# Optimization experiments

Hardware: AMD Instinct MI355X
Metric: run time of the kernel (lower is better)

## Reference

```python
import jax, jax.numpy as jnp
import numpy as np
from jax import lax

B, C, H, W = 8, 128, 48, 48
N = H * W
SPARSITY = 0.8
K_TOP = int(N * SPARSITY)


def conv2d(x, w, b, padding, dilation=1):
    # x: [B,C,H,W], w: [O,I,kh,kw]
    out = lax.conv_general_dilated(
        x, w, window_strides=(1, 1),
        padding=[(padding, padding), (padding, padding)],
        rhs_dilation=(dilation, dilation),
        dimension_numbers=('NCHW', 'OIHW', 'NCHW'))
    return out + b[None, :, None, None]


def setup_inputs() -> dict:
    key = jax.random.key(0)
    ks = jax.random.split(key, 16)
    s = 0.02
    return {
        'x': jax.random.normal(ks[0], (B, C, H, W), jnp.float32),
        'prev_features': jax.random.normal(ks[1], (B, C, H, W), jnp.float32),
        'Wq': jax.random.normal(ks[2], (C, C), jnp.float32) * s,
        'bq': jnp.zeros((C,), jnp.float32),
        'Wk': jax.random.normal(ks[3], (C, C), jnp.float32) * s,
        'bk': jnp.zeros((C,), jnp.float32),
        'Wv': jax.random.normal(ks[4], (C, C), jnp.float32) * s,
        'bv': jnp.zeros((C,), jnp.float32),
        'ref_w': jax.random.normal(ks[5], (C, C, 3, 3), jnp.float32) * s,
        'ref_b': jnp.zeros((C,), jnp.float32),
        'gate_w': jax.random.normal(ks[6], (1, C, 3, 3), jnp.float32) * s,
        'gate_b': jnp.zeros((1,), jnp.float32),
        'cov_w': jax.random.normal(ks[7], (C, C, 3, 3), jnp.float32) * s,
        'cov_b': jnp.zeros((C,), jnp.float32),
    }


def reference(x, prev_features, Wq, bq, Wk, bk, Wv, bv,
              ref_w, ref_b, gate_w, gate_b, cov_w, cov_b):
    b_, c_, h_, w_ = x.shape
    n_ = h_ * w_
    # torch x.view(B, -1, C): raw reshape of NCHW memory (NOT a transpose)
    t = x.reshape(b_, n_, c_)
    # Linear layers (torch: y = x @ W.T + b)
    Q = t @ Wq.T + bq
    Kt = (t @ Wk.T + bk).transpose(0, 2, 1)  # [B,C,N]
    V = t @ Wv.T + bv
    attn = jnp.einsum('bnc,bcm->bnm', Q, Kt) / (c_ ** 0.5)  # [B,N,N]
    # top-k masking with scatter, as in the original
    _, idx = lax.top_k(attn, K_TOP)  # [B,N,k]
    bi = jnp.arange(b_)[:, None, None]
    ni = jnp.arange(n_)[None, :, None]
    mask = jnp.zeros_like(attn).at[bi, ni, idx].set(1.0)
    attn = attn * mask - 1e10 * (1.0 - mask)
    attn = jax.nn.softmax(attn, axis=-1)
    out = jnp.einsum('bnm,bmc->bnc', attn, V)  # [B,N,C]
    # torch view([B, C, sqrt(N), sqrt(N)]): raw reshape
    xs = out.reshape(b_, c_, h_, w_)
    # localized refinement
    importance = jax.nn.sigmoid(conv2d(xs, gate_w, gate_b, padding=1))
    xr = conv2d(xs * importance, ref_w, ref_b, padding=1)
    xs = xs + xr
    # temporal propagation
    xs = xs + 0.5 * prev_features
    # fast coverage conv: kernel 3, dilation 2, padding = 1 + 2 - 1 = 2
    return conv2d(xs, cov_w, cov_b, padding=2, dilation=2)
```

## Files before the change

### kernel.cpp

```cpp
#include <hip/hip_runtime.h>
#include <hip/hip_bf16.h>
#include <math.h>

#define BB 8
#define CC 128
#define NTOK 2304
#define KTOP 1843

typedef unsigned short u16;
typedef unsigned int   u32;
typedef __attribute__((ext_vector_type(8))) short short8;
typedef __attribute__((ext_vector_type(4))) float f32x4;

static __device__ __forceinline__ float bf2f(u16 u) {
    return __uint_as_float(((u32)u) << 16);
}
static __device__ __forceinline__ u16 f2bf(float f) {
    u32 x = __float_as_uint(f);
    return (u16)((x + 0x7fffu + ((x >> 16) & 1u)) >> 16);
}
static __device__ __forceinline__ float key2val(int k) {
    u32 raw = (k & 0x8000) ? (u32)(k ^ 0x8000) : ((~(u32)k) & 0xFFFFu);
    return __uint_as_float(raw << 16);
}

__global__ __launch_bounds__(256) void qkv_kernel(
    const float* __restrict__ x,
    const float* __restrict__ Wq, const float* __restrict__ bq,
    const float* __restrict__ Wk, const float* __restrict__ bk,
    const float* __restrict__ Wv, const float* __restrict__ bv,
    u16* __restrict__ q_ws, u16* __restrict__ k_ws, u16* __restrict__ v_ws)
{
    __shared__ float t_lds[128 * 68];
    __shared__ u16 st[64 * 128];
    int blk = blockIdx.x;
    int b  = blk / 36;
    int n0 = (blk % 36) * 64;
    int tid = threadIdx.x;
    const float* xb = x + (size_t)(b * NTOK + n0) * CC;
    #pragma unroll
    for (int k = 0; k < 32; ++k) {
        int idx = k * 256 + tid;
        t_lds[(idx & 127) * 68 + (idx >> 7)] = xb[idx];
    }
    __syncthreads();
    int o  = tid & 127;
    int rh = tid >> 7;
    const float* Ws[3] = {Wq, Wk, Wv};
    const float* bs[3] = {bq, bk, bv};
    for (int mat = 0; mat < 3; ++mat) {
        const float* W = Ws[mat];
        float acc[32];
        #pragma unroll
        for (int j = 0; j < 32; ++j) acc[j] = 0.f;
        for (int c = 0; c < 128; ++c) {
            float w = W[o * 128 + c];
            const float4* t4p = (const float4*)&t_lds[c * 68 + rh * 32];
            #pragma unroll
            for (int j4 = 0; j4 < 8; ++j4) {
                float4 t4 = t4p[j4];
                acc[j4*4+0] += t4.x * w;
                acc[j4*4+1] += t4.y * w;
                acc[j4*4+2] += t4.z * w;
                acc[j4*4+3] += t4.w * w;
            }
        }
        float bias = bs[mat][o];
        if (mat == 2) {
            ushort4* vp4 = (ushort4*)(v_ws + (size_t)(b * CC + o) * NTOK + n0 + rh * 32);
            #pragma unroll
            for (int j8 = 0; j8 < 8; ++j8) {
                ushort4 s;
                s.x = f2bf(acc[j8*4+0] + bias); s.y = f2bf(acc[j8*4+1] + bias);
                s.z = f2bf(acc[j8*4+2] + bias); s.w = f2bf(acc[j8*4+3] + bias);
                vp4[j8] = s;
            }
        } else {
            float sc = (mat == 0) ? 0.08838834764831845f : 1.0f;
            #pragma unroll
            for (int j = 0; j < 32; ++j)
                st[(rh * 32 + j) * 128 + o] = f2bf((acc[j] + bias) * sc);
            __syncthreads();
            u16* gp = (mat == 0 ? q_ws : k_ws) + (size_t)(b * NTOK + n0) * CC;
            const ushort4* s4 = (const ushort4*)st;
            ushort4* g4 = (ushort4*)gp;
            for (int k = tid; k < 2048; k += 256) g4[k] = s4[k];
            __syncthreads();
        }
    }
}

__global__ __launch_bounds__(256) void qk_kernel(
    const u16* __restrict__ q_ws, const u16* __restrict__ k_ws,
    u16* __restrict__ sc)
{
    int tid = threadIdx.x;
    int lane = tid & 63, wid = tid >> 6;
    int blk = blockIdx.x;
    int b = blk & 7;
    int t = blk >> 3;
    int qt = t % 36, mt = t / 36;
    int q0 = qt * 64 + wid * 16;
    int m0 = mt * 64;
    int fr = lane & 15, fg = lane >> 4;

    const u16* qb = q_ws + (size_t)(b * NTOK + q0 + fr) * CC + fg * 8;
    short8 qa[4];
    #pragma unroll
    for (int kc = 0; kc < 4; ++kc) qa[kc] = *(const short8*)(qb + kc * 32);

    const u16* kb = k_ws + (size_t)(b * NTOK + m0 + fr) * CC + fg * 8;
    f32x4 acc[4];
    #pragma unroll
    for (int i = 0; i < 4; ++i) acc[i] = (f32x4){0.f, 0.f, 0.f, 0.f};
    #pragma unroll
    for (int mt2 = 0; mt2 < 4; ++mt2) {
        const u16* kp = kb + (size_t)(mt2 * 16) * CC;
        #pragma unroll
        for (int kc = 0; kc < 4; ++kc) {
            short8 kf = *(const short8*)(kp + kc * 32);
            acc[mt2] = __builtin_amdgcn_mfma_f32_16x16x32_bf16(qa[kc], kf, acc[mt2], 0, 0, 0);
        }
    }
    #pragma unroll
    for (int mt2 = 0; mt2 < 4; ++mt2) {
        #pragma unroll
        for (int r = 0; r < 4; ++r) {
            int row = q0 + fg * 4 + r;
            int col = m0 + mt2 * 16 + fr;
            u16 raw = f2bf(acc[mt2][r]);
            u16 key = (raw & 0x8000u) ? (u16)~raw : (u16)(raw | 0x8000u);
            sc[((size_t)b * NTOK + row) * NTOK + col] = key;
        }
    }
}

__global__ __launch_bounds__(256) void topk_kernel(
    u16* __restrict__ sc, float* __restrict__ rowinv)
{
    int tid = threadIdx.x;
    int lane = tid & 63, wid = tid >> 6;
    size_t rg0 = (size_t)blockIdx.x * 8 + wid * 2;
    u16* s0 = sc + rg0 * NTOK;
    u16* s1 = s0 + NTOK;

    int keys0[36], keys1[36];
    int kmax0 = 0, kmax1 = 0;
    #pragma unroll
    for (int j = 0; j < 9; ++j) {
        ushort4 a = *(const ushort4*)(s0 + j * 256 + lane * 4);
        ushort4 c = *(const ushort4*)(s1 + j * 256 + lane * 4);
        keys0[j*4+0] = a.x; keys0[j*4+1] = a.y; keys0[j*4+2] = a.z; keys0[j*4+3] = a.w;
        keys1[j*4+0] = c.x; keys1[j*4+1] = c.y; keys1[j*4+2] = c.z; keys1[j*4+3] = c.w;
        kmax0 = max(kmax0, max(max((int)a.x, (int)a.y), max((int)a.z, (int)a.w)));
        kmax1 = max(kmax1, max(max((int)c.x, (int)c.y), max((int)c.z, (int)c.w)));
    }
    #pragma unroll
    for (int off = 32; off; off >>= 1) {
        kmax0 = max(kmax0, __shfl_xor(kmax0, off, 64));
        kmax1 = max(kmax1, __shfl_xor(kmax1, off, 64));
    }
    u32 res0 = 0, res1 = 0;
    for (int bit = 15; bit >= 0; --bit) {
        int cand0 = (int)(res0 | (1u << bit));
        int cand1 = (int)(res1 | (1u << bit));
        int c0 = 0, c1 = 0;
        #pragma unroll
        for (int j = 0; j < 36; ++j) {
            c0 += (keys0[j] >= cand0) ? 1 : 0;
            c1 += (keys1[j] >= cand1) ? 1 : 0;
        }
        #pragma unroll
        for (int off = 32; off; off >>= 1) {
            c0 += __shfl_xor(c0, off, 64);
            c1 += __shfl_xor(c1, off, 64);
        }
        if (c0 >= KTOP) res0 = (u32)cand0;
        if (c1 >= KTOP) res1 = (u32)cand1;
    }
    float vmax0 = key2val(kmax0), vmax1 = key2val(kmax1);
    float sum0 = 0.f, sum1 = 0.f;
    #pragma unroll
    for (int j = 0; j < 9; ++j) {
        ushort4 w0, w1;
        float e;
        e = ((u32)keys0[j*4+0] >= res0) ? __expf(key2val(keys0[j*4+0]) - vmax0) : 0.f; sum0 += e; w0.x = f2bf(e);
        e = ((u32)keys0[j*4+1] >= res0) ? __expf(key2val(keys0[j*4+1]) - vmax0) : 0.f; sum0 += e; w0.y = f2bf(e);
        e = ((u32)keys0[j*4+2] >= res0) ? __expf(key2val(keys0[j*4+2]) - vmax0) : 0.f; sum0 += e; w0.z = f2bf(e);
        e = ((u32)keys0[j*4+3] >= res0) ? __expf(key2val(keys0[j*4+3]) - vmax0) : 0.f; sum0 += e; w0.w = f2bf(e);
        e = ((u32)keys1[j*4+0] >= res1) ? __expf(key2val(keys1[j*4+0]) - vmax1) : 0.f; sum1 += e; w1.x = f2bf(e);
        e = ((u32)keys1[j*4+1] >= res1) ? __expf(key2val(keys1[j*4+1]) - vmax1) : 0.f; sum1 += e; w1.y = f2bf(e);
        e = ((u32)keys1[j*4+2] >= res1) ? __expf(key2val(keys1[j*4+2]) - vmax1) : 0.f; sum1 += e; w1.z = f2bf(e);
        e = ((u32)keys1[j*4+3] >= res1) ? __expf(key2val(keys1[j*4+3]) - vmax1) : 0.f; sum1 += e; w1.w = f2bf(e);
        *(ushort4*)(s0 + j * 256 + lane * 4) = w0;
        *(ushort4*)(s1 + j * 256 + lane * 4) = w1;
    }
    #pragma unroll
    for (int off = 32; off; off >>= 1) {
        sum0 += __shfl_xor(sum0, off, 64);
        sum1 += __shfl_xor(sum1, off, 64);
    }
    if (lane == 0) {
        rowinv[rg0]     = 1.f / sum0;
        rowinv[rg0 + 1] = 1.f / sum1;
    }
}

__global__ __launch_bounds__(256) void pv_kernel(
    const u16* __restrict__ sc, const u16* __restrict__ v_ws,
    const float* __restrict__ rowinv, float* __restrict__ xs_ws)
{
    int tid = threadIdx.x;
    int lane = tid & 63, wid = tid >> 6;
    int blk = blockIdx.x;
    int b = blk & 7;
    int rt = blk >> 3;
    int r0 = rt * 32 + (wid & 1) * 16;
    int c0 = (wid >> 1) * 64;
    int fr = lane & 15, fg = lane >> 4;

    const u16* pb = sc + ((size_t)b * NTOK + r0 + fr) * NTOK + fg * 8;
    const u16* vb = v_ws + (size_t)(b * CC + c0 + fr) * NTOK + fg * 8;
    f32x4 acc[4];
    #pragma unroll
    for (int i = 0; i < 4; ++i) acc[i] = (f32x4){0.f, 0.f, 0.f, 0.f};
    for (int ch = 0; ch < 72; ++ch) {
        int m0 = ch * 32;
        short8 pa = *(const short8*)(pb + m0);
        #pragma unroll
        for (int t = 0; t < 4; ++t) {
            short8 vf = *(const short8*)(vb + (size_t)t * 16 * NTOK + m0);
            acc[t] = __builtin_amdgcn_mfma_f32_16x16x32_bf16(pa, vf, acc[t], 0, 0, 0);
        }
    }
    #pragma unroll
    for (int r = 0; r < 4; ++r) {
        int row = r0 + fg * 4 + r;
        float inv = rowinv[(size_t)b * NTOK + row];
        float* op = xs_ws + ((size_t)b * NTOK + row) * CC + c0;
        #pragma unroll
        for (int t = 0; t < 4; ++t) op[t * 16 + fr] = acc[t][r] * inv;
    }
}

__global__ __launch_bounds__(256) void gate_kernel(
    const float* __restrict__ xs_ws, const float* __restrict__ gw,
    const float* __restrict__ gb, float* __restrict__ imp_ws)
{
    __shared__ float gsum[256];
    int blk = blockIdx.x;
    int b  = blk & 7;
    int p0 = (blk >> 3) * 64;
    int tid = threadIdx.x;
    int pl = tid & 63, cq = tid >> 6;
    int p = p0 + pl;
    int h = p / 48, w = p % 48;
    float acc = 0.f;
    const float* xb = xs_ws + (size_t)b * CC * NTOK;
    for (int i = cq * 32; i < cq * 32 + 32; ++i) {
        const float* plane = xb + (size_t)i * NTOK;
        const float* wv = gw + i * 9;
        #pragma unroll
        for (int kh = 0; kh < 3; ++kh) {
            int hh = h + kh - 1;
            if ((unsigned)hh >= 48u) continue;
            #pragma unroll
            for (int kw = 0; kw < 3; ++kw) {
                int ww = w + kw - 1;
                if ((unsigned)ww >= 48u) continue;
                acc += plane[hh * 48 + ww] * wv[kh * 3 + kw];
            }
        }
    }
    gsum[cq * 64 + pl] = acc;
    __syncthreads();
    if (tid < 64) {
        float s = gsum[tid] + gsum[64 + tid] + gsum[128 + tid] + gsum[192 + tid] + gb[0];
        imp_ws[b * NTOK + p0 + tid] = 1.f / (1.f + __expf(-s));
    }
}

__global__ __launch_bounds__(256) void wtrans_kernel(
    const float* __restrict__ rw, const float* __restrict__ cw,
    u16* __restrict__ wb_ref, u16* __restrict__ wb_cov)
{
    int idx = blockIdx.x * 256 + threadIdx.x;
    int which = idx >= 147456;
    int rem = which ? idx - 147456 : idx;
    int tap = rem >> 14;
    int rest = rem & 16383;
    int o = rest >> 7, c = rest & 127;
    const float* src = which ? cw : rw;
    u16* dst = which ? wb_cov : wb_ref;
    dst[rem] = f2bf(src[(o * 128 + c) * 9 + tap]);
}

__global__ __launch_bounds__(256) void tpos_kernel(
    const float* __restrict__ xs_ws, const float* __restrict__ prev,
    const float* __restrict__ imp_ws,
    u16* __restrict__ xt_g, float* __restrict__ rbuf)
{
    __shared__ float tx[128 * 65];
    __shared__ float tp[128 * 65];
    int blk = blockIdx.x;
    int b  = blk & 7;
    int p0 = (blk >> 3) * 64;
    int tid = threadIdx.x;
    const float* xsb = xs_ws + (size_t)b * CC * NTOK + p0;
    const float* pvb = prev  + (size_t)b * CC * NTOK + p0;
    #pragma unroll
    for (int it = 0; it < 32; ++it) {
        int idx = it * 256 + tid;
        int i = idx >> 6, pp = idx & 63;
        tx[i * 65 + pp] = xsb[(size_t)i * NTOK + pp];
        tp[i * 65 + pp] = pvb[(size_t)i * NTOK + pp];
    }
    __syncthreads();
    int pl = tid & 63, cq = tid >> 6;
    float impv = imp_ws[b * NTOK + p0 + pl];
    size_t obase = ((size_t)b * NTOK + p0 + pl) * CC + cq * 32;
    u16* gout = xt_g + obase;
    float* rout = rbuf + obase;
    #pragma unroll
    for (int j4 = 0; j4 < 8; ++j4) {
        float4 rv; ushort4 gv;
        float v0 = tx[(cq * 32 + j4 * 4 + 0) * 65 + pl];
        float v1 = tx[(cq * 32 + j4 * 4 + 1) * 65 + pl];
        float v2 = tx[(cq * 32 + j4 * 4 + 2) * 65 + pl];
        float v3 = tx[(cq * 32 + j4 * 4 + 3) * 65 + pl];
        float q0 = tp[(cq * 32 + j4 * 4 + 0) * 65 + pl];
        float q1 = tp[(cq * 32 + j4 * 4 + 1) * 65 + pl];
        float q2 = tp[(cq * 32 + j4 * 4 + 2) * 65 + pl];
        float q3 = tp[(cq * 32 + j4 * 4 + 3) * 65 + pl];
        rv.x = v0 + 0.5f * q0; rv.y = v1 + 0.5f * q1;
        rv.z = v2 + 0.5f * q2; rv.w = v3 + 0.5f * q3;
        gv.x = f2bf(v0 * impv); gv.y = f2bf(v1 * impv);
        gv.z = f2bf(v2 * impv); gv.w = f2bf(v3 * impv);
        *(float4*)(rout + j4 * 4) = rv;
        *(ushort4*)(gout + j4 * 4) = gv;
    }
}

__global__ __launch_bounds__(256) void refgemm_kernel(
    const u16* __restrict__ xt_g, const u16* __restrict__ wb_ref,
    const float* __restrict__ rbuf, const float* __restrict__ rb,
    u16* __restrict__ xt2)
{
    __shared__ u16 slab[144 * 128];
    int tid = threadIdx.x;
    int lane = tid & 63, wid = tid >> 6;
    int blk = blockIdx.x;
    int b  = blk & 7;
    int st = (blk >> 3) & 15;
    int oh = blk >> 7;
    int h0 = st * 3;
    int p0g = st * 144;
    int fr = lane & 15, fg = lane >> 4;
    int o0 = oh * 64 + wid * 16;
    const u16* xb = xt_g + (size_t)b * NTOK * CC;

    f32x4 acc[9];
    #pragma unroll
    for (int pt = 0; pt < 9; ++pt) acc[pt] = (f32x4){0.f, 0.f, 0.f, 0.f};

    for (int tap = 0; tap < 9; ++tap) {
        int dh = tap / 3 - 1, dw = tap % 3 - 1;
        __syncthreads();
        #pragma unroll
        for (int it = 0; it < 9; ++it) {
            int idx = it * 256 + tid;
            int pr = idx >> 4, cv = idx & 15;
            int r = pr >= 96 ? 2 : (pr >= 48 ? 1 : 0);
            int w = pr - r * 48;
            int sh = h0 + r + dh, sw = w + dw;
            short8 val = (short8){0,0,0,0,0,0,0,0};
            if ((unsigned)sh < 48u && (unsigned)sw < 48u)
                val = *(const short8*)(xb + (size_t)(sh * 48 + sw) * CC + cv * 8);
            *(short8*)(slab + pr * 128 + ((cv ^ (pr & 7)) * 8)) = val;
        }
        __syncthreads();
        #pragma unroll
        for (int kc = 0; kc < 4; ++kc) {
            short8 bfr = *(const short8*)(wb_ref + tap * 16384 + (o0 + fr) * 128 + kc * 32 + fg * 8);
            #pragma unroll
            for (int pt = 0; pt < 9; ++pt) {
                int prr = pt * 16 + fr;
                short8 pa = *(const short8*)(slab + prr * 128 + (((kc * 4 + fg) ^ (prr & 7)) * 8));
                acc[pt] = __builtin_amdgcn_mfma_f32_16x16x32_bf16(pa, bfr, acc[pt], 0, 0, 0);
            }
        }
    }
    int o = o0 + fr;
    float bias = rb[o];
    #pragma unroll
    for (int pt = 0; pt < 9; ++pt) {
        #pragma unroll
        for (int r = 0; r < 4; ++r) {
            int p = p0g + pt * 16 + fg * 4 + r;
            size_t off = ((size_t)b * NTOK + p) * CC + o;
            float v = acc[pt][r] + bias + rbuf[off];
            xt2[off] = f2bf(v);
        }
    }
}

__global__ __launch_bounds__(256) void covgemm_kernel(
    const u16* __restrict__ xt2, const u16* __restrict__ wb_cov,
    const float* __restrict__ cb, float* __restrict__ out)
{
    __shared__ u16 slab[144 * 128];
    __shared__ float ldsout[4 * 16 * 145];
    int tid = threadIdx.x;
    int lane = tid & 63, wid = tid >> 6;
    int blk = blockIdx.x;
    int b  = blk & 7;
    int st = (blk >> 3) & 15;
    int oh = blk >> 7;
    int h0 = st * 3;
    int p0g = st * 144;
    int fr = lane & 15, fg = lane >> 4;
    int o0 = oh * 64 + wid * 16;
    const u16* xb = xt2 + (size_t)b * NTOK * CC;

    f32x4 acc[9];
    #pragma unroll
    for (int pt = 0; pt < 9; ++pt) acc[pt] = (f32x4){0.f, 0.f, 0.f, 0.f};

    for (int tap = 0; tap < 9; ++tap) {
        int dh = (tap / 3 - 1) * 2, dw = (tap % 3 - 1) * 2;
        __syncthreads();
        #pragma unroll
        for (int it = 0; it < 9; ++it) {
            int idx = it * 256 + tid;
            int pr = idx >> 4, cv = idx & 15;
            int r = pr >= 96 ? 2 : (pr >= 48 ? 1 : 0);
            int w = pr - r * 48;
            int sh = h0 + r + dh, sw = w + dw;
            short8 val = (short8){0,0,0,0,0,0,0,0};
            if ((unsigned)sh < 48u && (unsigned)sw < 48u)
                val = *(const short8*)(xb + (size_t)(sh * 48 + sw) * CC + cv * 8);
            *(short8*)(slab + pr * 128 + ((cv ^ (pr & 7)) * 8)) = val;
        }
        __syncthreads();
        #pragma unroll
        for (int kc = 0; kc < 4; ++kc) {
            short8 bfr = *(const short8*)(wb_cov + tap * 16384 + (o0 + fr) * 128 + kc * 32 + fg * 8);
            #pragma unroll
            for (int pt = 0; pt < 9; ++pt) {
                int prr = pt * 16 + fr;
                short8 pa = *(const short8*)(slab + prr * 128 + (((kc * 4 + fg) ^ (prr & 7)) * 8));
                acc[pt] = __builtin_amdgcn_mfma_f32_16x16x32_bf16(pa, bfr, acc[pt], 0, 0, 0);
            }
        }
    }
    float bias = cb[o0 + fr];
    float* lo = ldsout + wid * (16 * 145);
    #pragma unroll
    for (int pt = 0; pt < 9; ++pt) {
        #pragma unroll
        for (int r = 0; r < 4; ++r) {
            int pl = pt * 16 + fg * 4 + r;
            lo[fr * 145 + pl] = acc[pt][r] + bias;
        }
    }
    __syncthreads();
    float* ob = out + ((size_t)b * CC + o0) * NTOK + p0g;
    #pragma unroll
    for (int j = 0; j < 36; ++j) {
        int idx = j * 64 + lane;
        int o_r = idx / 144;
        int p_r = idx - o_r * 144;
        ob[(size_t)o_r * NTOK + p_r] = lo[o_r * 145 + p_r];
    }
}

extern "C" void kernel_launch(void* const* d_in, const int* in_sizes, int n_in,
                              void* d_out, int out_size, void* d_ws, size_t ws_size,
                              hipStream_t stream)
{
    const float* x    = (const float*)d_in[0];
    const float* prev = (const float*)d_in[1];
    const float* Wq   = (const float*)d_in[2];
    const float* bq   = (const float*)d_in[3];
    const float* Wk   = (const float*)d_in[4];
    const float* bk   = (const float*)d_in[5];
    const float* Wv   = (const float*)d_in[6];
    const float* bv   = (const float*)d_in[7];
    const float* rw   = (const float*)d_in[8];
    const float* rb   = (const float*)d_in[9];
    const float* gw   = (const float*)d_in[10];
    const float* gb   = (const float*)d_in[11];
    const float* cw   = (const float*)d_in[12];
    const float* cb   = (const float*)d_in[13];
    float* out = (float*)d_out;
    char* ws = (char*)d_ws;

    const size_t SZ  = (size_t)BB * NTOK * CC;
    const size_t BSZ = SZ * 2;
    const size_t FSZ = SZ * 4;
    const size_t SCB = (size_t)BB * NTOK * NTOK * 2;
    const size_t RIB = (size_t)BB * NTOK * 4;

    u16*   q_ws   = (u16*)(ws);
    u16*   k_ws   = (u16*)(ws + BSZ);
    u16*   v_ws   = (u16*)(ws + 2 * BSZ);
    u16*   sc_ws  = (u16*)(ws + 3 * BSZ);
    float* ri_ws  = (float*)(ws + 3 * BSZ + SCB);
    float* xs_ws  = (float*)(ws + 3 * BSZ + SCB + RIB);
    float* imp_ws = (float*)(ws + 3 * BSZ + SCB + RIB + FSZ);
    u16*   xt_g   = (u16*)(ws + 3 * BSZ + SCB + 2 * RIB + FSZ);
    float* rbuf   = (float*)(ws + 4 * BSZ + SCB + 2 * RIB + FSZ);
    u16*   xt2    = (u16*)(ws + 4 * BSZ + SCB + 2 * RIB + 2 * FSZ);
    u16*   wb_ref = (u16*)(ws + 5 * BSZ + SCB + 2 * RIB + 2 * FSZ);
    u16*   wb_cov = (u16*)(ws + 5 * BSZ + SCB + 2 * RIB + 2 * FSZ + 294912);

    qkv_kernel<<<dim3(288), dim3(256), 0, stream>>>(x, Wq, bq, Wk, bk, Wv, bv,
                                                    q_ws, k_ws, v_ws);
    qk_kernel<<<dim3(10368), dim3(256), 0, stream>>>(q_ws, k_ws, sc_ws);
    topk_kernel<<<dim3(2304), dim3(256), 0, stream>>>(sc_ws, ri_ws);
    pv_kernel<<<dim3(576), dim3(256), 0, stream>>>(sc_ws, v_ws, ri_ws, xs_ws);
    gate_kernel<<<dim3(288), dim3(256), 0, stream>>>(xs_ws, gw, gb, imp_ws);
    wtrans_kernel<<<dim3(1152), dim3(256), 0, stream>>>(rw, cw, wb_ref, wb_cov);
    tpos_kernel<<<dim3(288), dim3(256), 0, stream>>>(xs_ws, prev, imp_ws, xt_g, rbuf);
    refgemm_kernel<<<dim3(256), dim3(256), 0, stream>>>(xt_g, wb_ref, rbuf, rb, xt2);
    covgemm_kernel<<<dim3(256), dim3(256), 0, stream>>>(xt2, wb_cov, cb, out);
}
```

Before: 570.1 us.

## Fuse softmax exp into PV kernel, write only per-row top-k params

The top-k kernel no longer rewrites the full bf16 score matrix with exponentiated probabilities. It stores only a per-row threshold, max and inverse sum. The PV kernel reads the raw score keys, applies the threshold and exp on the fly, and feeds the result to MFMA. Each PV wave now covers all 128 channels, so each score row is read once instead of twice. This removes a full write pass over the large score matrix and duplicate reads, at the cost of extra exp work inside the PV loop and fewer waves per block.

```diff
diff --git a/kernel.cpp b/kernel.cpp
--- a/kernel.cpp
+++ b/kernel.cpp
@@ -136,13 +136,13 @@
 }
 
 __global__ __launch_bounds__(256) void topk_kernel(
-    u16* __restrict__ sc, float* __restrict__ rowinv)
+    const u16* __restrict__ sc, float4* __restrict__ params)
 {
     int tid = threadIdx.x;
     int lane = tid & 63, wid = tid >> 6;
     size_t rg0 = (size_t)blockIdx.x * 8 + wid * 2;
-    u16* s0 = sc + rg0 * NTOK;
-    u16* s1 = s0 + NTOK;
+    const u16* s0 = sc + rg0 * NTOK;
+    const u16* s1 = s0 + NTOK;
 
     int keys0[36], keys1[36];
     int kmax0 = 0, kmax1 = 0;
@@ -181,19 +181,9 @@
     float vmax0 = key2val(kmax0), vmax1 = key2val(kmax1);
     float sum0 = 0.f, sum1 = 0.f;
     #pragma unroll
-    for (int j = 0; j < 9; ++j) {
-        ushort4 w0, w1;
-        float e;
-        e = ((u32)keys0[j*4+0] >= res0) ? __expf(key2val(keys0[j*4+0]) - vmax0) : 0.f; sum0 += e; w0.x = f2bf(e);
-        e = ((u32)keys0[j*4+1] >= res0) ? __expf(key2val(keys0[j*4+1]) - vmax0) : 0.f; sum0 += e; w0.y = f2bf(e);
-        e = ((u32)keys0[j*4+2] >= res0) ? __expf(key2val(keys0[j*4+2]) - vmax0) : 0.f; sum0 += e; w0.z = f2bf(e);
-        e = ((u32)keys0[j*4+3] >= res0) ? __expf(key2val(keys0[j*4+3]) - vmax0) : 0.f; sum0 += e; w0.w = f2bf(e);
-        e = ((u32)keys1[j*4+0] >= res1) ? __expf(key2val(keys1[j*4+0]) - vmax1) : 0.f; sum1 += e; w1.x = f2bf(e);
-        e = ((u32)keys1[j*4+1] >= res1) ? __expf(key2val(keys1[j*4+1]) - vmax1) : 0.f; sum1 += e; w1.y = f2bf(e);
-        e = ((u32)keys1[j*4+2] >= res1) ? __expf(key2val(keys1[j*4+2]) - vmax1) : 0.f; sum1 += e; w1.z = f2bf(e);
-        e = ((u32)keys1[j*4+3] >= res1) ? __expf(key2val(keys1[j*4+3]) - vmax1) : 0.f; sum1 += e; w1.w = f2bf(e);
-        *(ushort4*)(s0 + j * 256 + lane * 4) = w0;
-        *(ushort4*)(s1 + j * 256 + lane * 4) = w1;
+    for (int j = 0; j < 36; ++j) {
+        if ((u32)keys0[j] >= res0) sum0 += __expf(key2val(keys0[j]) - vmax0);
+        if ((u32)keys1[j] >= res1) sum1 += __expf(key2val(keys1[j]) - vmax1);
     }
     #pragma unroll
     for (int off = 32; off; off >>= 1) {
@@ -201,45 +191,60 @@
         sum1 += __shfl_xor(sum1, off, 64);
     }
     if (lane == 0) {
-        rowinv[rg0]     = 1.f / sum0;
-        rowinv[rg0 + 1] = 1.f / sum1;
-    }
-}
-
-__global__ __launch_bounds__(256) void pv_kernel(
+        params[rg0]     = make_float4(__uint_as_float(res0), vmax0, 1.f / sum0, 0.f);
+        params[rg0 + 1] = make_float4(__uint_as_float(res1), vmax1, 1.f / sum1, 0.f);
+    }
+}
+
+__global__ __launch_bounds__(128) void pv_kernel(
     const u16* __restrict__ sc, const u16* __restrict__ v_ws,
-    const float* __restrict__ rowinv, float* __restrict__ xs_ws)
+    const float4* __restrict__ params, float* __restrict__ xs_ws)
 {
     int tid = threadIdx.x;
     int lane = tid & 63, wid = tid >> 6;
     int blk = blockIdx.x;
     int b = blk & 7;
     int rt = blk >> 3;
-    int r0 = rt * 32 + (wid & 1) * 16;
-    int c0 = (wid >> 1) * 64;
+    int r0 = rt * 32 + wid * 16;
     int fr = lane & 15, fg = lane >> 4;
-
-    const u16* pb = sc + ((size_t)b * NTOK + r0 + fr) * NTOK + fg * 8;
-    const u16* vb = v_ws + (size_t)(b * CC + c0 + fr) * NTOK + fg * 8;
-    f32x4 acc[4];
-    #pragma unroll
-    for (int i = 0; i < 4; ++i) acc[i] = (f32x4){0.f, 0.f, 0.f, 0.f};
+    int row = r0 + fr;
+
+    float4 pr = params[(size_t)b * NTOK + row];
+    u32 res = __float_as_uint(pr.x);
+    float vmax = pr.y;
+
+    const u16* kb = sc + ((size_t)b * NTOK + row) * NTOK + fg * 8;
+    const u16* vb = v_ws + ((size_t)b * CC + fr) * NTOK + fg * 8;
+
+    f32x4 acc[8];
+    #pragma unroll
+    for (int i = 0; i < 8; ++i) acc[i] = (f32x4){0.f, 0.f, 0.f, 0.f};
+
+    #pragma unroll 2
     for (int ch = 0; ch < 72; ++ch) {
         int m0 = ch * 32;
-        short8 pa = *(const short8*)(pb + m0);
-        #pragma unroll
-        for (int t = 0; t < 4; ++t) {
-            short8 vf = *(const short8*)(vb + (size_t)t * 16 * NTOK + m0);
+        short8 kv = *(const short8*)(kb + m0);
+        short8 pa;
+        #pragma unroll
+        for (int j = 0; j < 8; ++j) {
+            int k = (int)(u16)kv[j];
+            float e = 0.f;
+            if ((u32)k >= res) e = __expf(key2val(k) - vmax);
+            pa[j] = (short)f2bf(e);
+        }
+        #pragma unroll
+        for (int t = 0; t < 8; ++t) {
+            short8 vf = *(const short8*)(vb + (size_t)(t * 16) * NTOK + m0);
             acc[t] = __builtin_amdgcn_mfma_f32_16x16x32_bf16(pa, vf, acc[t], 0, 0, 0);
         }
     }
     #pragma unroll
     for (int r = 0; r < 4; ++r) {
-        int row = r0 + fg * 4 + r;
-        float inv = rowinv[(size_t)b * NTOK + row];
-        float* op = xs_ws + ((size_t)b * NTOK + row) * CC + c0;
-        #pragma unroll
-        for (int t = 0; t < 4; ++t) op[t * 16 + fr] = acc[t][r] * inv;
+        int orow = r0 + fg * 4 + r;
+        float inv = params[(size_t)b * NTOK + orow].z;
+        float* op = xs_ws + ((size_t)b * NTOK + orow) * CC;
+        #pragma unroll
+        for (int t = 0; t < 8; ++t) op[t * 16 + fr] = acc[t][r] * inv;
     }
 }
 
@@ -499,26 +504,28 @@
     const size_t BSZ = SZ * 2;
     const size_t FSZ = SZ * 4;
     const size_t SCB = (size_t)BB * NTOK * NTOK * 2;
+    const size_t PRB = (size_t)BB * NTOK * 16;
     const size_t RIB = (size_t)BB * NTOK * 4;
 
-    u16*   q_ws   = (u16*)(ws);
-    u16*   k_ws   = (u16*)(ws + BSZ);
-    u16*   v_ws   = (u16*)(ws + 2 * BSZ);
-    u16*   sc_ws  = (u16*)(ws + 3 * BSZ);
-    float* ri_ws  = (float*)(ws + 3 * BSZ + SCB);
-    float* xs_ws  = (float*)(ws + 3 * BSZ + SCB + RIB);
-    float* imp_ws = (float*)(ws + 3 * BSZ + SCB + RIB + FSZ);
-    u16*   xt_g   = (u16*)(ws + 3 * BSZ + SCB + 2 * RIB + FSZ);
-    float* rbuf   = (float*)(ws + 4 * BSZ + SCB + 2 * RIB + FSZ);
-    u16*   xt2    = (u16*)(ws + 4 * BSZ + SCB + 2 * RIB + 2 * FSZ);
-    u16*   wb_ref = (u16*)(ws + 5 * BSZ + SCB + 2 * RIB + 2 * FSZ);
-    u16*   wb_cov = (u16*)(ws + 5 * BSZ + SCB + 2 * RIB + 2 * FSZ + 294912);
+    size_t off = 0;
+    u16*    q_ws   = (u16*)(ws + off);    off += BSZ;
+    u16*    k_ws   = (u16*)(ws + off);    off += BSZ;
+    u16*    v_ws   = (u16*)(ws + off);    off += BSZ;
+    u16*    sc_ws  = (u16*)(ws + off);    off += SCB;
+    float4* prm_ws = (float4*)(ws + off); off += PRB;
+    float*  xs_ws  = (float*)(ws + off);  off += FSZ;
+    float*  imp_ws = (float*)(ws + off);  off += RIB;
+    u16*    xt_g   = (u16*)(ws + off);    off += BSZ;
+    float*  rbuf   = (float*)(ws + off);  off += FSZ;
+    u16*    xt2    = (u16*)(ws + off);    off += BSZ;
+    u16*    wb_ref = (u16*)(ws + off);    off += 294912;
+    u16*    wb_cov = (u16*)(ws + off);    off += 294912;
 
     qkv_kernel<<<dim3(288), dim3(256), 0, stream>>>(x, Wq, bq, Wk, bk, Wv, bv,
                                                     q_ws, k_ws, v_ws);
     qk_kernel<<<dim3(10368), dim3(256), 0, stream>>>(q_ws, k_ws, sc_ws);
-    topk_kernel<<<dim3(2304), dim3(256), 0, stream>>>(sc_ws, ri_ws);
-    pv_kernel<<<dim3(576), dim3(256), 0, stream>>>(sc_ws, v_ws, ri_ws, xs_ws);
+    topk_kernel<<<dim3(2304), dim3(256), 0, stream>>>(sc_ws, prm_ws);
+    pv_kernel<<<dim3(576), dim3(128), 0, stream>>>(sc_ws, v_ws, prm_ws, xs_ws);
     gate_kernel<<<dim3(288), dim3(256), 0, stream>>>(xs_ws, gw, gb, imp_ws);
     wtrans_kernel<<<dim3(1152), dim3(256), 0, stream>>>(rw, cw, wb_ref, wb_cov);
     tpos_kernel<<<dim3(288), dim3(256), 0, stream>>>(xs_ws, prev, imp_ws, xt_g, rbuf);
```

Result: no change. 567.7 us (-0.4%).
